# Optimization experiments

Hardware: AMD Instinct MI355X
Metric: run time of the kernel (lower is better)

The kernel has to match this reference:

```python
import jax, jax.numpy as jnp
import numpy as np

D_MODEL, HIDDEN, H, NB = 1024, 128, 16, 32
B, L = 4, 4096


def setup_inputs() -> dict:
    key = jax.random.key(0)
    ks = jax.random.split(key, 6)
    theta_path = jax.random.normal(ks[0], (B, L, H, NB), dtype=jnp.float32)
    content_emb = jax.random.normal(ks[1], (B, L, D_MODEL), dtype=jnp.float32)
    # params (log_Pi init 0.0; final linear weight scaled by 0.01, bias 0, as in torch init)
    log_Pi = jnp.zeros((H, NB), dtype=jnp.float32)
    W1 = jax.random.normal(ks[2], (D_MODEL, HIDDEN), dtype=jnp.float32) / np.sqrt(D_MODEL)
    b1 = jnp.zeros((HIDDEN,), dtype=jnp.float32)
    W2 = (jax.random.normal(ks[3], (HIDDEN, H * NB), dtype=jnp.float32) / np.sqrt(HIDDEN)) * 0.01
    b2 = jnp.zeros((H * NB,), dtype=jnp.float32)
    return {"theta_path": theta_path, "content_emb": content_emb,
            "log_Pi": log_Pi, "W1": W1, "b1": b1, "W2": W2, "b2": b2}


def _affine_combine(c1, c2):
    a1, u1 = c1
    a2, u2 = c2
    return a2 * a1, a2 * u1 + u2


def reference(theta_path, content_emb, log_Pi, W1, b1, W2, b2):
    Bx, Lx, Hx, NBx = theta_path.shape
    # log_R_head: Linear -> GELU(exact) -> Linear, then clamp
    h = jax.nn.gelu(content_emb @ W1 + b1, approximate=False)
    log_R = jnp.clip((h @ W2 + b2).reshape(Bx, Lx, Hx, NBx), -5.0, 5.0)
    R = jnp.exp(log_R)
    # wrapped innovation nu = atan2(sin(-theta), cos(-theta))
    nu = jnp.arctan2(jnp.sin(-theta_path), jnp.cos(-theta_path))
    Pi = jnp.exp(log_Pi)[None, None]            # [1,1,H,NB]
    K = Pi / jnp.maximum(Pi + R, 1e-8)
    alpha = 1.0 - K
    u = K * nu
    # affine recurrence d_t = alpha_t * d_{t-1} + u_t, parallel scan over L
    _, d = jax.lax.associative_scan(_affine_combine, (alpha, u), axis=1)
    return theta_path + d, jnp.broadcast_to(Pi, R.shape), K, R
```

## Files before the change

### kernel.cpp

```cpp
#include <hip/hip_runtime.h>
#include <math.h>

#define B_   4
#define L_   4096
#define C_   512
#define DM_  1024
#define HID_ 128
#define M_   (B_*L_)
#define NC_  256
#define CT_  16

typedef __attribute__((ext_vector_type(8))) short short8;
typedef __attribute__((ext_vector_type(4))) float f32x4;
typedef __attribute__((ext_vector_type(2))) float f32x2;

__device__ __forceinline__ unsigned short f2bf(float f) {
  unsigned u = __float_as_uint(f);
  u += 0x7fffu + ((u >> 16) & 1u);
  return (unsigned short)(u >> 16);
}

__device__ __forceinline__ float wrap_neg(float th) {
  return 6.283185307179586f * rintf(th * 0.15915494309189535f) - th;
}

__global__ __launch_bounds__(256) void k_prep(const float* __restrict__ W1,
                                              const float* __restrict__ W2,
                                              unsigned short* __restrict__ W1T,
                                              unsigned short* __restrict__ W2T) {
  int idx = blockIdx.x * 256 + threadIdx.x;
  if (idx < DM_ * HID_) {
    int n = idx >> 10, k = idx & 1023;
    W1T[idx] = f2bf(W1[(size_t)k * HID_ + n]);
  }
  int i2 = idx - DM_ * HID_;
  if (i2 >= 0 && i2 < HID_ * C_) {
    int n = i2 >> 7, k = i2 & 127;
    W2T[i2] = f2bf(W2[(size_t)k * C_ + n]);
  }
}

__global__ __launch_bounds__(512) void k_mlp(const float* __restrict__ X,
                                             const unsigned short* __restrict__ W1T,
                                             const float* __restrict__ b1,
                                             const unsigned short* __restrict__ W2T,
                                             const float* __restrict__ b2,
                                             unsigned short* __restrict__ logRq) {
  __shared__ char lds[49152];
  const int tid  = threadIdx.x;
  const int m0   = blockIdx.x * 32;
  const int lane = tid & 63;
  const int wave = tid >> 6;
  const int wr   = wave >> 2;
  const int wc   = wave & 3;
  const int fr   = lane & 15;
  const int kg   = lane >> 4;

  f32x4 acc[2];
  acc[0] = (f32x4){0.f, 0.f, 0.f, 0.f};
  acc[1] = (f32x4){0.f, 0.f, 0.f, 0.f};

#define STAGE1(bufi, k0)                                                           \
  {                                                                                \
    if (tid < 256) {                                                               \
      int row = tid >> 3, k8 = tid & 7;                                            \
      const f32x4* src = (const f32x4*)(X + (size_t)(m0 + row) * DM_ + (k0) + k8 * 8); \
      f32x4 v0 = __builtin_nontemporal_load(src);                                  \
      f32x4 v1 = __builtin_nontemporal_load(src + 1);                              \
      uint4 pk;                                                                    \
      pk.x = f2bf(v0[0]) | ((unsigned)f2bf(v0[1]) << 16);                          \
      pk.y = f2bf(v0[2]) | ((unsigned)f2bf(v0[3]) << 16);                          \
      pk.z = f2bf(v1[0]) | ((unsigned)f2bf(v1[1]) << 16);                          \
      pk.w = f2bf(v1[2]) | ((unsigned)f2bf(v1[3]) << 16);                          \
      *(uint4*)(lds + (bufi) * 4096 + row * 128 + ((k8 ^ (row & 7)) << 4)) = pk;   \
    }                                                                              \
    _Pragma("unroll")                                                              \
    for (int t = 0; t < 2; ++t) {                                                  \
      int c = tid + t * 512;                                                       \
      int n = c >> 3, k8 = c & 7;                                                  \
      uint4 v = *(const uint4*)(W1T + (size_t)n * DM_ + (k0) + k8 * 8);            \
      *(uint4*)(lds + 8192 + (bufi) * 16384 + n * 128 + ((k8 ^ (n & 7)) << 4)) = v;\
    }                                                                              \
  }

  STAGE1(0, 0);
  __syncthreads();
  for (int it = 0; it < 16; ++it) {
    const int cur = it & 1;
    if (it < 15) STAGE1(1 - cur, (it + 1) * 64);
#pragma unroll
    for (int ks = 0; ks < 2; ++ks) {
      int row = wr * 16 + fr;
      short8 a = *(const short8*)(lds + cur * 4096 + row * 128 +
                                  (((ks * 4 + kg) ^ (row & 7)) << 4));
#pragma unroll
      for (int j = 0; j < 2; ++j) {
        int col = wc * 32 + j * 16 + fr;
        short8 b = *(const short8*)(lds + 8192 + cur * 16384 + col * 128 +
                                    (((ks * 4 + kg) ^ (col & 7)) << 4));
        acc[j] = __builtin_amdgcn_mfma_f32_16x16x32_bf16(a, b, acc[j], 0, 0, 0);
      }
    }
    __syncthreads();
  }
#pragma unroll
  for (int j = 0; j < 2; ++j) {
    int col = wc * 32 + j * 16 + fr;
    float bb = b1[col];
#pragma unroll
    for (int r = 0; r < 4; ++r) {
      int row = wr * 16 + kg * 4 + r;
      float x = acc[j][r] + bb;
      float g = 0.5f * x * (1.0f + erff(x * 0.70710678f));
      *(unsigned short*)(lds + 40960 + row * 256 +
                         (((col >> 3) ^ (row & 15)) << 4) + ((col & 7) << 1)) = f2bf(g);
    }
  }

#define STAGE2(bufi, nc)                                                           \
  {                                                                                \
    _Pragma("unroll")                                                              \
    for (int t = 0; t < 2; ++t) {                                                  \
      int c = tid + t * 512;                                                       \
      int n = c >> 4, k8 = c & 15;                                                 \
      uint4 v = *(const uint4*)(W2T + (size_t)((nc) * 64 + n) * HID_ + k8 * 8);    \
      *(uint4*)(lds + (bufi) * 16384 + n * 256 + ((k8 ^ (n & 15)) << 4)) = v;      \
    }                                                                              \
  }

  STAGE2(0, 0);
  __syncthreads();
  for (int nc = 0; nc < 8; ++nc) {
    const int cur = nc & 1;
    if (nc < 7) STAGE2(1 - cur, nc + 1);

    f32x4 a2 = (f32x4){0.f, 0.f, 0.f, 0.f};
#pragma unroll
    for (int ks = 0; ks < 4; ++ks) {
      int row = wr * 16 + fr;
      short8 af = *(const short8*)(lds + 40960 + row * 256 +
                                   (((ks * 4 + kg) ^ (row & 15)) << 4));
      int col = wc * 16 + fr;
      short8 bf2 = *(const short8*)(lds + cur * 16384 + col * 256 +
                                    (((ks * 4 + kg) ^ (col & 15)) << 4));
      a2 = __builtin_amdgcn_mfma_f32_16x16x32_bf16(af, bf2, a2, 0, 0, 0);
    }
    {
      int col = nc * 64 + wc * 16 + fr;
      float bb = b2[col];
#pragma unroll
      for (int r = 0; r < 4; ++r) {
        int row = m0 + wr * 16 + kg * 4 + r;
        float lr = a2[r] + bb;
        lr = fminf(5.0f, fmaxf(-5.0f, lr));
        logRq[(size_t)row * C_ + col] = (unsigned short)rintf((lr + 5.0f) * 6553.5f);
      }
    }
    __syncthreads();
  }
}

__global__ __launch_bounds__(256) void k_epi(const unsigned short* __restrict__ logRq,
                                             const float* __restrict__ logPi,
                                             const float* __restrict__ theta,
                                             float* __restrict__ out1,
                                             float* __restrict__ out2,
                                             float* __restrict__ out3,
                                             float* __restrict__ Ab,
                                             float* __restrict__ Ub) {
  const int blk = blockIdx.x;
  const int b   = blk >> 8;
  const int ch  = blk & 255;
  const int c0  = threadIdx.x * 2;
  const float Pi0 = expf(logPi[c0]);
  const float Pi1 = expf(logPi[c0 + 1]);
  const size_t rowbase = ((size_t)b * L_ + (size_t)ch * CT_) * C_;
  float A0 = 1.f, U0 = 0.f, A1 = 1.f, U1 = 0.f;
  const float dq = 1.0f / 6553.5f;
#pragma unroll
  for (int j = 0; j < CT_; ++j) {
    size_t o = rowbase + (size_t)j * C_ + c0;
    unsigned q = *(const unsigned*)(logRq + o);
    f32x2 th = *(const f32x2*)(theta + o);
    float lr0 = (float)(q & 0xffffu) * dq - 5.0f;
    float lr1 = (float)(q >> 16) * dq - 5.0f;
    float R0 = expf(lr0), R1 = expf(lr1);
    float K0 = Pi0 / fmaxf(Pi0 + R0, 1e-8f);
    float K1 = Pi1 / fmaxf(Pi1 + R1, 1e-8f);
    f32x2 p2 = {Pi0, Pi1}, k2 = {K0, K1}, r2 = {R0, R1};
    __builtin_nontemporal_store(p2, (f32x2*)(out1 + o));
    *(f32x2*)(out2 + o) = k2;
    __builtin_nontemporal_store(r2, (f32x2*)(out3 + o));
    float nu0 = wrap_neg(th[0]), nu1 = wrap_neg(th[1]);
    float a0 = 1.f - K0, a1 = 1.f - K1;
    U0 = a0 * U0 + K0 * nu0; A0 *= a0;
    U1 = a1 * U1 + K1 * nu1; A1 *= a1;
  }
  size_t co = ((size_t)(b * NC_ + ch)) * C_ + c0;
  f32x2 A2 = {A0, A1}, U2 = {U0, U1};
  *(f32x2*)(Ab + co) = A2;
  *(f32x2*)(Ub + co) = U2;
}

__global__ __launch_bounds__(256) void k_scan2(const float* __restrict__ Ab,
                                               const float* __restrict__ Ub,
                                               float* __restrict__ D0) {
  __shared__ float cA[16][17], cU[16][17], carry[16][17];
  const int tid = threadIdx.x;
  const int b   = blockIdx.x >> 5;
  const int c0  = (blockIdx.x & 31) * 16;
  const int c_l = tid & 15, s = tid >> 4;
  const int c   = c0 + c_l;
  float A = 1.f, U = 0.f;
#pragma unroll
  for (int k = 0; k < 16; ++k) {
    size_t o = ((size_t)(b * NC_ + s * 16 + k)) * C_ + c;
    float a = Ab[o], u = Ub[o];
    U = a * U + u; A *= a;
  }
  cA[s][c_l] = A; cU[s][c_l] = U;
  __syncthreads();
  if (tid < 16) {
    float P = 0.f;
#pragma unroll
    for (int ss = 0; ss < 16; ++ss) {
      carry[ss][tid] = P;
      P = cA[ss][tid] * P + cU[ss][tid];
    }
  }
  __syncthreads();
  float d = carry[s][c_l];
#pragma unroll
  for (int k = 0; k < 16; ++k) {
    size_t o = ((size_t)(b * NC_ + s * 16 + k)) * C_ + c;
    D0[o] = d;
    d = Ab[o] * d + Ub[o];
  }
}

__global__ __launch_bounds__(256) void k_scan3(const float* __restrict__ Kv,
                                               const float* __restrict__ theta,
                                               const float* __restrict__ D0,
                                               float* __restrict__ out0) {
  const int b  = blockIdx.x / NC_;
  const int ch = blockIdx.x % NC_;
  const int c  = blockIdx.y * 256 + threadIdx.x;
  size_t base = ((size_t)b * L_ + (size_t)ch * CT_) * C_ + c;
  float d = D0[((size_t)(b * NC_ + ch)) * C_ + c];
#pragma unroll 4
  for (int j = 0; j < CT_; ++j) {
    size_t idx = base + (size_t)j * C_;
    float k  = Kv[idx];
    float th = theta[idx];
    float nu = wrap_neg(th);
    d = (1.f - k) * d + k * nu;
    __builtin_nontemporal_store(th + d, &out0[idx]);
  }
}

extern "C" void kernel_launch(void* const* d_in, const int* in_sizes, int n_in,
                              void* d_out, int out_size, void* d_ws, size_t ws_size,
                              hipStream_t stream) {
  const float* theta = (const float*)d_in[0];
  const float* X     = (const float*)d_in[1];
  const float* logPi = (const float*)d_in[2];
  const float* W1    = (const float*)d_in[3];
  const float* b1    = (const float*)d_in[4];
  const float* W2    = (const float*)d_in[5];
  const float* b2    = (const float*)d_in[6];

  float* out = (float*)d_out;
  const size_t S = (size_t)M_ * C_;
  float* out0 = out;
  float* out1 = out + S;
  float* out2 = out + 2 * S;
  float* out3 = out + 3 * S;

  unsigned short* W1T   = (unsigned short*)d_ws;
  unsigned short* W2T   = W1T + (size_t)DM_ * HID_;
  unsigned short* logRq = W2T + (size_t)HID_ * C_;
  float* Ab = (float*)(logRq + S);
  float* Ub = Ab + (size_t)B_ * NC_ * C_;
  float* D0 = Ub + (size_t)B_ * NC_ * C_;

  hipLaunchKernelGGL(k_prep, dim3(768), dim3(256), 0, stream, W1, W2, W1T, W2T);
  hipLaunchKernelGGL(k_mlp, dim3(M_ / 32), dim3(512), 0, stream,
                     X, W1T, b1, W2T, b2, logRq);
  hipLaunchKernelGGL(k_epi, dim3(B_ * NC_), dim3(256), 0, stream,
                     logRq, logPi, theta, out1, out2, out3, Ab, Ub);
  hipLaunchKernelGGL(k_scan2, dim3(B_ * 32), dim3(256), 0, stream, Ab, Ub, D0);
  hipLaunchKernelGGL(k_scan3, dim3(B_ * NC_, 2), dim3(256), 0, stream, out2, theta, D0, out0);
}
```

Measured before the change: 86.85 us.

## Store local scan prefix and product as packed bf16 to simplify final scan pass

The epilogue now computes, for each element, the within-chunk cumulative decay product and theta plus the local prefix, and stores both packed as bf16 in one 32-bit word. The final pass then becomes an elementwise fused multiply-add with the chunk carry, reading only 4 bytes per element instead of re-reading K and theta (8 bytes) and running a serial recurrence. Chunks shrink to 8 rows with 4-wide vectorized loads and stores, and the carry scan is adjusted to handle twice as many chunks. The trade-off is an extra 4-byte intermediate write per element and reduced precision, since the cumulative product and sum are rounded to bf16.

Measured after the change: 93.27 us. 1.07x slower.

```diff
diff --git a/kernel.cpp b/kernel.cpp
--- a/kernel.cpp
+++ b/kernel.cpp
@@ -7,17 +7,19 @@
 #define DM_  1024
 #define HID_ 128
 #define M_   (B_*L_)
-#define NC_  256
-#define CT_  16
+#define NC_  512
+#define CT_  8
 
 typedef __attribute__((ext_vector_type(8))) short short8;
 typedef __attribute__((ext_vector_type(4))) float f32x4;
-typedef __attribute__((ext_vector_type(2))) float f32x2;
 
 __device__ __forceinline__ unsigned short f2bf(float f) {
   unsigned u = __float_as_uint(f);
   u += 0x7fffu + ((u >> 16) & 1u);
   return (unsigned short)(u >> 16);
+}
+__device__ __forceinline__ float bf2f(unsigned v) {
+  return __uint_as_float(v << 16);
 }
 
 __device__ __forceinline__ float wrap_neg(float th) {
@@ -166,40 +168,57 @@
                                              float* __restrict__ out1,
                                              float* __restrict__ out2,
                                              float* __restrict__ out3,
+                                             unsigned* __restrict__ ASq,
                                              float* __restrict__ Ab,
                                              float* __restrict__ Ub) {
   const int blk = blockIdx.x;
   const int b   = blk >> 8;
-  const int ch  = blk & 255;
-  const int c0  = threadIdx.x * 2;
-  const float Pi0 = expf(logPi[c0]);
-  const float Pi1 = expf(logPi[c0 + 1]);
-  const size_t rowbase = ((size_t)b * L_ + (size_t)ch * CT_) * C_;
-  float A0 = 1.f, U0 = 0.f, A1 = 1.f, U1 = 0.f;
+  const int cb  = blk & 255;
+  const int g   = threadIdx.x & 127;
+  const int h   = threadIdx.x >> 7;
+  const int c0  = g * 4;
+  const int row0 = cb * 16 + h * 8;
+  const int ch   = cb * 2 + h;
+
+  f32x4 lp = *(const f32x4*)(logPi + c0);
+  f32x4 Pi4;
+#pragma unroll
+  for (int q = 0; q < 4; ++q) Pi4[q] = expf(lp[q]);
+
+  f32x4 A4 = {1.f, 1.f, 1.f, 1.f}, U4 = {0.f, 0.f, 0.f, 0.f};
   const float dq = 1.0f / 6553.5f;
+  const size_t base = ((size_t)b * L_ + row0) * C_ + c0;
 #pragma unroll
   for (int j = 0; j < CT_; ++j) {
-    size_t o = rowbase + (size_t)j * C_ + c0;
-    unsigned q = *(const unsigned*)(logRq + o);
-    f32x2 th = *(const f32x2*)(theta + o);
-    float lr0 = (float)(q & 0xffffu) * dq - 5.0f;
-    float lr1 = (float)(q >> 16) * dq - 5.0f;
-    float R0 = expf(lr0), R1 = expf(lr1);
-    float K0 = Pi0 / fmaxf(Pi0 + R0, 1e-8f);
-    float K1 = Pi1 / fmaxf(Pi1 + R1, 1e-8f);
-    f32x2 p2 = {Pi0, Pi1}, k2 = {K0, K1}, r2 = {R0, R1};
-    __builtin_nontemporal_store(p2, (f32x2*)(out1 + o));
-    *(f32x2*)(out2 + o) = k2;
-    __builtin_nontemporal_store(r2, (f32x2*)(out3 + o));
-    float nu0 = wrap_neg(th[0]), nu1 = wrap_neg(th[1]);
-    float a0 = 1.f - K0, a1 = 1.f - K1;
-    U0 = a0 * U0 + K0 * nu0; A0 *= a0;
-    U1 = a1 * U1 + K1 * nu1; A1 *= a1;
+    size_t o = base + (size_t)j * C_;
+    uint2 q2 = *(const uint2*)(logRq + o);
+    f32x4 th = *(const f32x4*)(theta + o);
+    float lr[4] = { (float)(q2.x & 0xffffu) * dq - 5.0f,
+                    (float)(q2.x >> 16)     * dq - 5.0f,
+                    (float)(q2.y & 0xffffu) * dq - 5.0f,
+                    (float)(q2.y >> 16)     * dq - 5.0f };
+    f32x4 R4, K4;
+    uint4 pk;
+#pragma unroll
+    for (int q = 0; q < 4; ++q) {
+      float R = expf(lr[q]);
+      float K = Pi4[q] / fmaxf(Pi4[q] + R, 1e-8f);
+      R4[q] = R; K4[q] = K;
+      float nu = wrap_neg(th[q]);
+      float a = 1.f - K;
+      U4[q] = a * U4[q] + K * nu;
+      A4[q] *= a;
+      float s = th[q] + U4[q];
+      (&pk.x)[q] = (unsigned)f2bf(A4[q]) | ((unsigned)f2bf(s) << 16);
+    }
+    __builtin_nontemporal_store(Pi4, (f32x4*)(out1 + o));
+    __builtin_nontemporal_store(K4,  (f32x4*)(out2 + o));
+    __builtin_nontemporal_store(R4,  (f32x4*)(out3 + o));
+    *(uint4*)(ASq + o) = pk;
   }
   size_t co = ((size_t)(b * NC_ + ch)) * C_ + c0;
-  f32x2 A2 = {A0, A1}, U2 = {U0, U1};
-  *(f32x2*)(Ab + co) = A2;
-  *(f32x2*)(Ub + co) = U2;
+  *(f32x4*)(Ab + co) = A4;
+  *(f32x4*)(Ub + co) = U4;
 }
 
 __global__ __launch_bounds__(256) void k_scan2(const float* __restrict__ Ab,
@@ -212,9 +231,9 @@
   const int c_l = tid & 15, s = tid >> 4;
   const int c   = c0 + c_l;
   float A = 1.f, U = 0.f;
-#pragma unroll
-  for (int k = 0; k < 16; ++k) {
-    size_t o = ((size_t)(b * NC_ + s * 16 + k)) * C_ + c;
+#pragma unroll 4
+  for (int k = 0; k < 32; ++k) {
+    size_t o = ((size_t)(b * NC_ + s * 32 + k)) * C_ + c;
     float a = Ab[o], u = Ub[o];
     U = a * U + u; A *= a;
   }
@@ -230,32 +249,31 @@
   }
   __syncthreads();
   float d = carry[s][c_l];
-#pragma unroll
-  for (int k = 0; k < 16; ++k) {
-    size_t o = ((size_t)(b * NC_ + s * 16 + k)) * C_ + c;
+#pragma unroll 4
+  for (int k = 0; k < 32; ++k) {
+    size_t o = ((size_t)(b * NC_ + s * 32 + k)) * C_ + c;
     D0[o] = d;
     d = Ab[o] * d + Ub[o];
   }
 }
 
-__global__ __launch_bounds__(256) void k_scan3(const float* __restrict__ Kv,
-                                               const float* __restrict__ theta,
+__global__ __launch_bounds__(256) void k_scan3(const unsigned* __restrict__ ASq,
                                                const float* __restrict__ D0,
                                                float* __restrict__ out0) {
-  const int b  = blockIdx.x / NC_;
-  const int ch = blockIdx.x % NC_;
-  const int c  = blockIdx.y * 256 + threadIdx.x;
-  size_t base = ((size_t)b * L_ + (size_t)ch * CT_) * C_ + c;
-  float d = D0[((size_t)(b * NC_ + ch)) * C_ + c];
-#pragma unroll 4
-  for (int j = 0; j < CT_; ++j) {
-    size_t idx = base + (size_t)j * C_;
-    float k  = Kv[idx];
-    float th = theta[idx];
-    float nu = wrap_neg(th);
-    d = (1.f - k) * d + k * nu;
-    __builtin_nontemporal_store(th + d, &out0[idx]);
-  }
+  size_t e = ((size_t)blockIdx.x * 256 + threadIdx.x) * 4;
+  int row = (int)(e >> 9);
+  int c0  = (int)(e & 511);
+  int b   = row >> 12, l = row & 4095;
+  int chk = l >> 3;
+  uint4 q = *(const uint4*)(ASq + e);
+  f32x4 d0 = *(const f32x4*)(D0 + (((size_t)(b * NC_ + chk)) << 9) + c0);
+  f32x4 o;
+#pragma unroll
+  for (int i = 0; i < 4; ++i) {
+    unsigned v = (&q.x)[i];
+    o[i] = bf2f(v >> 16) + bf2f(v & 0xffffu) * d0[i];
+  }
+  __builtin_nontemporal_store(o, (f32x4*)(out0 + e));
 }
 
 extern "C" void kernel_launch(void* const* d_in, const int* in_sizes, int n_in,
@@ -279,15 +297,16 @@
   unsigned short* W1T   = (unsigned short*)d_ws;
   unsigned short* W2T   = W1T + (size_t)DM_ * HID_;
   unsigned short* logRq = W2T + (size_t)HID_ * C_;
-  float* Ab = (float*)(logRq + S);
+  unsigned* ASq = (unsigned*)(logRq + S);
+  float* Ab = (float*)(ASq + S);
   float* Ub = Ab + (size_t)B_ * NC_ * C_;
   float* D0 = Ub + (size_t)B_ * NC_ * C_;
 
   hipLaunchKernelGGL(k_prep, dim3(768), dim3(256), 0, stream, W1, W2, W1T, W2T);
   hipLaunchKernelGGL(k_mlp, dim3(M_ / 32), dim3(512), 0, stream,
                      X, W1T, b1, W2T, b2, logRq);
-  hipLaunchKernelGGL(k_epi, dim3(B_ * NC_), dim3(256), 0, stream,
-                     logRq, logPi, theta, out1, out2, out3, Ab, Ub);
+  hipLaunchKernelGGL(k_epi, dim3(B_ * 256), dim3(256), 0, stream,
+                     logRq, logPi, theta, out1, out2, out3, ASq, Ab, Ub);
   hipLaunchKernelGGL(k_scan2, dim3(B_ * 32), dim3(256), 0, stream, Ab, Ub, D0);
-  hipLaunchKernelGGL(k_scan3, dim3(B_ * NC_, 2), dim3(256), 0, stream, out2, theta, D0, out0);
-}
+  hipLaunchKernelGGL(k_scan3, dim3((int)(S / 1024)), dim3(256), 0, stream, ASq, D0, out0);
+}
```
